# Optimization experiments

Hardware: AMD Instinct MI355X
Metric: run time of the kernel (lower is better)

## Reference

```python
import jax, jax.numpy as jnp
import numpy as np

H = W = 64          # input_resolution
C = 256             # dim
HEADS = 8
WS = 8              # window_size
SHIFT = WS // 2
DEPTH = 2           # block 0: no shift, block 1: shifted + mask
HIDDEN = 4 * C      # mlp_ratio * dim
B = 8
N = WS * WS                 # tokens per window
NW = (H // WS) * (W // WS)  # windows per image
EPS = 1e-5


def _rel_pos_index():
    coords = np.stack(np.meshgrid(np.arange(WS), np.arange(WS), indexing='ij')).reshape(2, -1)
    rel = (coords[:, :, None] - coords[:, None, :]).transpose(1, 2, 0)
    rel[:, :, 0] += WS - 1
    rel[:, :, 1] += WS - 1
    rel[:, :, 0] *= 2 * WS - 1
    return rel.sum(-1)  # [N, N] indices into (2*ws-1)^2 table

REL_IDX = jnp.asarray(_rel_pos_index())


def _attn_mask():
    # Swin shift mask: label 3x3 regions, compare window-token labels
    img = np.zeros((H, W))
    slices = (slice(0, -WS), slice(-WS, -SHIFT), slice(-SHIFT, None))
    cnt = 0
    for hs in slices:
        for ws_ in slices:
            img[hs, ws_] = cnt
            cnt += 1
    mw = img.reshape(H // WS, WS, W // WS, WS).transpose(0, 2, 1, 3).reshape(-1, N)
    diff = mw[:, None, :] - mw[:, :, None]
    return jnp.asarray(np.where(diff != 0, -100.0, 0.0), dtype=np.float32)  # [nW, N, N]

ATTN_MASK = _attn_mask()


def layernorm(x, g, b):
    mu = jnp.mean(x, axis=-1, keepdims=True)
    var = jnp.mean((x - mu) ** 2, axis=-1, keepdims=True)
    return (x - mu) * jax.lax.rsqrt(var + EPS) * g + b


def setup_inputs() -> dict:
    key = jax.random.key(0)
    ks = jax.random.split(key, 6)
    s = 0.02
    return {
        'x': jax.random.normal(ks[0], (B, H * W, C), jnp.float32),
        'qkv_w': jax.random.normal(ks[1], (DEPTH, C, 3 * C), jnp.float32) * s,
        'qkv_b': jnp.zeros((DEPTH, 3 * C), jnp.float32),
        'proj_w': jax.random.normal(ks[2], (DEPTH, C, C), jnp.float32) * s,
        'proj_b': jnp.zeros((DEPTH, C), jnp.float32),
        'ln1_g': jnp.ones((DEPTH, C), jnp.float32),
        'ln1_b': jnp.zeros((DEPTH, C), jnp.float32),
        'ln2_g': jnp.ones((DEPTH, C), jnp.float32),
        'ln2_b': jnp.zeros((DEPTH, C), jnp.float32),
        'fc1_w': jax.random.normal(ks[3], (DEPTH, C, HIDDEN), jnp.float32) * s,
        'fc1_b': jnp.zeros((DEPTH, HIDDEN), jnp.float32),
        'fc2_w': jax.random.normal(ks[4], (DEPTH, HIDDEN, C), jnp.float32) * s,
        'fc2_b': jnp.zeros((DEPTH, C), jnp.float32),
        'rpb': jax.random.normal(ks[5], (DEPTH, (2 * WS - 1) ** 2, HEADS), jnp.float32) * s,
    }


def window_attention(xw, qw, qb, pw, pb, rpb_i, mask):
    # xw: [B*nW, N, C]
    B_ = xw.shape[0]
    d = C // HEADS
    qkv = (xw @ qw + qb).reshape(B_, N, 3, HEADS, d).transpose(2, 0, 3, 1, 4)
    q, k, v = qkv[0] * (d ** -0.5), qkv[1], qkv[2]   # [B_, h, N, d]
    attn = jnp.einsum('bhnd,bhmd->bhnm', q, k)
    bias = rpb_i[REL_IDX.reshape(-1)].reshape(N, N, HEADS).transpose(2, 0, 1)
    attn = attn + bias[None]
    if mask is not None:
        attn = attn.reshape(-1, NW, HEADS, N, N) + mask[None, :, None]
        attn = attn.reshape(-1, HEADS, N, N)
    attn = jax.nn.softmax(attn, axis=-1)
    out = jnp.einsum('bhnm,bhmd->bhnd', attn, v).transpose(0, 2, 1, 3).reshape(B_, N, C)
    return out @ pw + pb


def reference(x, qkv_w, qkv_b, proj_w, proj_b, ln1_g, ln1_b, ln2_g, ln2_b,
              fc1_w, fc1_b, fc2_w, fc2_b, rpb):
    for i in range(DEPTH):
        shift = 0 if i % 2 == 0 else SHIFT
        mask = None if shift == 0 else ATTN_MASK
        shortcut = x
        h = layernorm(x, ln1_g[i], ln1_b[i]).reshape(-1, H, W, C)
        if shift:
            h = jnp.roll(h, (-shift, -shift), axis=(1, 2))
        # window partition -> [B*nW, N, C]
        hw = h.reshape(-1, H // WS, WS, W // WS, WS, C).transpose(0, 1, 3, 2, 4, 5).reshape(-1, N, C)
        aw = window_attention(hw, qkv_w[i], qkv_b[i], proj_w[i], proj_b[i], rpb[i], mask)
        # window reverse
        h = aw.reshape(-1, H // WS, W // WS, WS, WS, C).transpose(0, 1, 3, 2, 4, 5).reshape(-1, H, W, C)
        if shift:
            h = jnp.roll(h, (shift, shift), axis=(1, 2))
        x = shortcut + h.reshape(-1, H * W, C)
        m = layernorm(x, ln2_g[i], ln2_b[i])
        m = jax.nn.gelu(m @ fc1_w[i] + fc1_b[i], approximate=False) @ fc2_w[i] + fc2_b[i]
        x = x + m
    return x
```

## Files before the change

### kernel.cpp

```cpp
#include <hip/hip_runtime.h>
#include <hip/hip_bf16.h>


typedef __hip_bfloat16 bf16;
typedef unsigned short u16;
typedef unsigned int u32;
typedef short short8 __attribute__((ext_vector_type(8)));
typedef float floatx4 __attribute__((ext_vector_type(4)));

#define DEVI static __device__ __forceinline__
#define WAITCNT_VM(n) asm volatile("s_waitcnt vmcnt(" #n ")" ::: "memory")

DEVI float lo16(u32 u) { union { u32 i; float f; } x; x.i = u << 16; return x.f; }
DEVI float hi16(u32 u) { union { u32 i; float f; } x; x.i = u & 0xffff0000u; return x.f; }
DEVI float b2f(u16 u) { union { u32 i; float f; } x; x.i = ((u32)u) << 16; return x.f; }
DEVI u16 f2b(float f) {
  union { float f; u32 i; } x; x.f = f;
  u32 r = x.i + 0x7fffu + ((x.i >> 16) & 1u);
  return (u16)(r >> 16);
}
DEVI float in_elem(const void* p, size_t i, int m) {
  return m ? b2f(((const u16*)p)[i]) : ((const float*)p)[i];
}
DEVI int swlab(int g) { return (g < 56) ? 0 : (g < 60 ? 1 : 2); }

DEVI float gelu_cheap(float v) {
  const float u = v * v;
  const float t = v * __builtin_fmaf(0.1029436f, u, 2.3022090f);
  const float e = __builtin_amdgcn_exp2f(t);
  const float r = __builtin_amdgcn_rcpf(e + 1.0f);
  return __builtin_fmaf(-v, r, v);
}

DEVI void async16(const bf16* g, bf16* l) {
  __builtin_amdgcn_global_load_lds((const __attribute__((address_space(1))) u32*)g,
                                   (__attribute__((address_space(3))) u32*)l, 16, 0, 0);
}

__global__ void k_detect(const u32* __restrict__ ln1g, int* __restrict__ mode) {
  if (threadIdx.x == 0 && blockIdx.x == 0)
    *mode = (ln1g[0] == 0x3F803F80u) ? 1 : 0;
}

__global__ __launch_bounds__(256) void k_ingest_ln(const void* __restrict__ xin,
    float* __restrict__ xf, const void* __restrict__ gamw, const void* __restrict__ betw,
    bf16* __restrict__ outp, const int* __restrict__ mode)
{
  const int m = *mode;
  const int l = threadIdx.x & 63, w = threadIdx.x >> 6;
  const int row = blockIdx.x * 4 + w;
  const int t = row & 63, win = row >> 6;
  const int bb = win >> 6, wi = win & 63;
  const int gh = ((wi >> 3) << 3) + (t >> 3);
  const int gw = ((wi & 7) << 3) + (t & 7);
  const int srow = (bb << 12) + (gh << 6) + gw;
  const int cb = l << 2;
  float4 v;
  if (m) {
    const uint2 u = *(const uint2*)((const u16*)xin + (size_t)srow * 256 + cb);
    v = make_float4(lo16(u.x), hi16(u.x), lo16(u.y), hi16(u.y));
  } else {
    v = ((const float4*)((const float*)xin + (size_t)srow * 256))[l];
  }
  ((float4*)(xf + (size_t)srow * 256))[l] = v;
  float s = v.x + v.y + v.z + v.w;
#pragma unroll
  for (int off = 32; off > 0; off >>= 1) s += __shfl_xor(s, off, 64);
  const float mu = s * 0.00390625f;
  const float a = v.x - mu, b = v.y - mu, c = v.z - mu, d = v.w - mu;
  float q = a * a + b * b + c * c + d * d;
#pragma unroll
  for (int off = 32; off > 0; off >>= 1) q += __shfl_xor(q, off, 64);
  const float rs = rsqrtf(q * 0.00390625f + 1e-5f);
  const float o0 = a * rs * in_elem(gamw, cb + 0, m) + in_elem(betw, cb + 0, m);
  const float o1 = b * rs * in_elem(gamw, cb + 1, m) + in_elem(betw, cb + 1, m);
  const float o2 = c * rs * in_elem(gamw, cb + 2, m) + in_elem(betw, cb + 2, m);
  const float o3 = d * rs * in_elem(gamw, cb + 3, m) + in_elem(betw, cb + 3, m);
  const u32 p0 = (u32)f2b(o0) | ((u32)f2b(o1) << 16);
  const u32 p1 = (u32)f2b(o2) | ((u32)f2b(o3) << 16);
  *(uint2*)((u16*)outp + (size_t)row * 256 + cb) = make_uint2(p0, p1);
}

__global__ __launch_bounds__(256) void k_transpose(
    const void* __restrict__ src, bf16* __restrict__ dst,
    const int* __restrict__ mode, int estride, int dstride, int R, int Cn) {
  __shared__ float T[32][33];
  const int m = *mode;
  const int tx = threadIdx.x & 31, ty = threadIdx.x >> 5;
  const int bc = blockIdx.x << 5, br = blockIdx.y << 5;
  for (int d = 0; d < 2; ++d) {
    __syncthreads();
#pragma unroll
    for (int dy = 0; dy < 4; ++dy) {
      const int r = br + ty + dy * 8;
      T[ty + dy * 8][tx] = in_elem(src, (size_t)d * estride + (size_t)r * Cn + bc + tx, m);
    }
    __syncthreads();
#pragma unroll
    for (int dy = 0; dy < 4; ++dy) {
      const int c = bc + ty + dy * 8;
      ((u16*)dst)[(size_t)d * dstride + (size_t)c * R + br + tx] = f2b(T[tx][ty + dy * 8]);
    }
  }
}

template <int EPI>
__global__ __launch_bounds__(256, 3) void k_gemm(
    const bf16* __restrict__ A, const bf16* __restrict__ Bt,
    const void* __restrict__ bias, bf16* __restrict__ outb,
    const int* __restrict__ mode, int boff, int K, int N)
{
  __shared__ __align__(16) bf16 As[3][128 * 32];
  __shared__ __align__(16) bf16 Bs[3][128 * 32];
  __shared__ __align__(16) float EPs[4][4][72];
  const int md = *mode;
  const int tid = threadIdx.x;
  const int l = tid & 63, wid = tid >> 6;
  const int wr = wid >> 1, wc = wid & 1;

  const int gx = gridDim.x;
  const int nwg = gx * gridDim.y;
  int fid = blockIdx.y * gx + blockIdx.x;
  if (!(nwg & 7)) fid = (fid & 7) * (nwg >> 3) + (fid >> 3);
  const int row0 = (fid / gx) * 128;
  const int col0 = (fid % gx) * 128;

  const int lrow = l >> 2;
  const int lkof = (((l & 3) ^ ((l >> 3) & 3)) * 8);
  const int qsw  = (((l >> 4) ^ ((l >> 1) & 3)) * 8);

  floatx4 acc[4][4];
#pragma unroll
  for (int mi = 0; mi < 4; ++mi)
#pragma unroll
    for (int ni = 0; ni < 4; ++ni)
      acc[mi][ni] = (floatx4){0.f, 0.f, 0.f, 0.f};

  auto stage = [&](int b, int kbase) {
    const int kk = kbase + lkof;
#pragma unroll
    for (int c = 0; c < 2; ++c) {
      const int seg = c * 4 + wid;
      async16(A + (size_t)(row0 + seg * 16 + lrow) * K + kk, &As[b][seg * 512]);
      async16(Bt + (size_t)(col0 + seg * 16 + lrow) * K + kk, &Bs[b][seg * 512]);
    }
  };

  const int nsl = K >> 5;
  stage(0, 0);
  stage(1, 32);

  for (int s = 0; s < nsl; ++s) {
    const int cur = s % 3;
    if (s < nsl - 1) { WAITCNT_VM(4); }
    else            { WAITCNT_VM(0); }
    __builtin_amdgcn_s_barrier();
    if (s + 2 < nsl) stage((s + 2) % 3, (s + 2) * 32);

    short8 af[4], bq[4];
#pragma unroll
    for (int mi = 0; mi < 4; ++mi)
      af[mi] = *(const short8*)&As[cur][(wr * 64 + mi * 16 + (l & 15)) * 32 + qsw];
#pragma unroll
    for (int ni = 0; ni < 4; ++ni)
      bq[ni] = *(const short8*)&Bs[cur][(wc * 64 + ni * 16 + (l & 15)) * 32 + qsw];
#pragma unroll
    for (int mi = 0; mi < 4; ++mi)
#pragma unroll
      for (int ni = 0; ni < 4; ++ni)
        acc[mi][ni] = __builtin_amdgcn_mfma_f32_16x16x32_bf16(af[mi], bq[ni], acc[mi][ni], 0, 0, 0);
  }

  float* EPw = &EPs[wid][0][0];
  const int cl = l & 15, rq = l >> 4;
  const int colb = wc * 64 + cl * 4;
  float bias4[4];
#pragma unroll
  for (int i = 0; i < 4; ++i) bias4[i] = in_elem(bias, (size_t)boff + col0 + colb + i, md);

#pragma unroll
  for (int mi = 0; mi < 4; ++mi) {
#pragma unroll
    for (int r = 0; r < 4; ++r) {
#pragma unroll
      for (int ni = 0; ni < 4; ++ni)
        EPw[rq * 72 + ni * 16 + cl] = acc[mi][ni][r];
      const float4 av = *(const float4*)&EPw[rq * 72 + cl * 4];
      float v0 = av.x + bias4[0], v1 = av.y + bias4[1];
      float v2 = av.z + bias4[2], v3 = av.w + bias4[3];
      if (EPI == 1) {
        v0 = gelu_cheap(v0); v1 = gelu_cheap(v1);
        v2 = gelu_cheap(v2); v3 = gelu_cheap(v3);
      }
      const int row = row0 + wr * 64 + mi * 16 + rq * 4 + r;
      const u32 p0 = (u32)f2b(v0) | ((u32)f2b(v1) << 16);
      const u32 p1 = (u32)f2b(v2) | ((u32)f2b(v3) << 16);
      *(uint2*)((u16*)outb + (size_t)row * N + col0 + colb) = make_uint2(p0, p1);
    }
  }
}

template <int MODE>
__global__ __launch_bounds__(256, 2) void k_fullN(
    const bf16* __restrict__ A, const bf16* __restrict__ Bt,
    const void* __restrict__ bias, const void* __restrict__ lng,
    const void* __restrict__ lnb, void* __restrict__ outp,
    float* __restrict__ xf, const int* __restrict__ mode,
    int boff, int lnoff, int K, int shift)
{
  __shared__ __align__(16) char smem[61440];
  bf16* As = (bf16*)smem;
  bf16* Bs = (bf16*)(smem + 12288);
  const int md = *mode;
  const int tid = threadIdx.x;
  const int l = tid & 63, w = tid >> 6;

  int fid = blockIdx.x;
  const int nwg = gridDim.x;
  if (!(nwg & 7)) fid = (fid & 7) * (nwg >> 3) + (fid >> 3);
  const int row0 = fid * 64;

  const int lrow = l >> 2;
  const int lkof = (((l & 3) ^ ((l >> 3) & 3)) * 8);
  const int qsw  = (((l >> 4) ^ ((l >> 1) & 3)) * 8);

  floatx4 acc[16];
#pragma unroll
  for (int ni = 0; ni < 16; ++ni) acc[ni] = (floatx4){0.f, 0.f, 0.f, 0.f};

  auto stage = [&](int b, int kbase) {
    const int kk = kbase + lkof;
    async16(A + (size_t)(row0 + w * 16 + lrow) * K + kk, As + b * 2048 + w * 512);
#pragma unroll
    for (int c = 0; c < 4; ++c) {
      const int seg = c * 4 + w;
      async16(Bt + (size_t)(seg * 16 + lrow) * K + kk, Bs + b * 8192 + seg * 512);
    }
  };

  const int nsl = K >> 5;
  stage(0, 0);
  stage(1, 32);

  for (int s = 0; s < nsl; ++s) {
    const int cur = s % 3;
    if (s < nsl - 1) { WAITCNT_VM(5); }
    else            { WAITCNT_VM(0); }
    __builtin_amdgcn_s_barrier();
    if (s + 2 < nsl) stage((s + 2) % 3, (s + 2) * 32);

    const short8 af = *(const short8*)&As[cur * 2048 + (w * 16 + (l & 15)) * 32 + qsw];
#pragma unroll
    for (int ni = 0; ni < 16; ++ni) {
      const short8 bq = *(const short8*)&Bs[cur * 8192 + (ni * 16 + (l & 15)) * 32 + qsw];
      acc[ni] = __builtin_amdgcn_mfma_f32_16x16x32_bf16(af, bq, acc[ni], 0, 0, 0);
    }
  }

  __syncthreads();

  float* EPw = (float*)smem + w * 1088;
  const int cl = l & 15, rq = l >> 4;
  const int c4 = l * 4;

  float bias4[4], g4[4], b4[4];
#pragma unroll
  for (int i = 0; i < 4; ++i) bias4[i] = in_elem(bias, (size_t)boff + c4 + i, md);
#pragma unroll
  for (int i = 0; i < 4; ++i) {
    g4[i] = in_elem(lng, (size_t)lnoff + c4 + i, md);
    b4[i] = in_elem(lnb, (size_t)lnoff + c4 + i, md);
  }

  for (int r = 0; r < 4; ++r) {
#pragma unroll
    for (int ni = 0; ni < 16; ++ni)
      EPw[rq * 272 + ni * 16 + cl] = acc[ni][r];

#pragma unroll
    for (int g = 0; g < 4; ++g) {
      const int lrow_g = row0 + w * 16 + g * 4 + r;
      const float4 av = *(const float4*)&EPw[g * 272 + c4];

      const int t_ = lrow_g & 63, win = lrow_g >> 6;
      const int bb = win >> 6, wi2 = win & 63;
      int gh = ((wi2 >> 3) << 3) + (t_ >> 3);
      int gw = ((wi2 & 7) << 3) + (t_ & 7);
      gh = (gh + shift) & 63; gw = (gw + shift) & 63;
      const int resrow = (bb << 12) + (gh << 6) + gw;
      const int dstrow = resrow;

      const float4 xv = *(const float4*)(xf + (size_t)resrow * 256 + c4);
      float t0 = av.x + bias4[0] + xv.x;
      float t1 = av.y + bias4[1] + xv.y;
      float t2 = av.z + bias4[2] + xv.z;
      float t3 = av.w + bias4[3] + xv.w;

      float s = t0 + t1 + t2 + t3;
#pragma unroll
      for (int off = 32; off > 0; off >>= 1) s += __shfl_xor(s, off, 64);
      const float mu = s * 0.00390625f;
      const float d0 = t0 - mu, d1 = t1 - mu, d2 = t2 - mu, d3 = t3 - mu;
      float q = d0 * d0 + d1 * d1 + d2 * d2 + d3 * d3;
#pragma unroll
      for (int off = 32; off > 0; off >>= 1) q += __shfl_xor(q, off, 64);
      const float rs = rsqrtf(q * 0.00390625f + 1e-5f);

      *(float4*)(xf + (size_t)resrow * 256 + c4) = make_float4(t0, t1, t2, t3);
      const u32 p0 = (u32)f2b(d0 * rs * g4[0] + b4[0]) | ((u32)f2b(d1 * rs * g4[1] + b4[1]) << 16);
      const u32 p1 = (u32)f2b(d2 * rs * g4[2] + b4[2]) | ((u32)f2b(d3 * rs * g4[3] + b4[3]) << 16);
      *(uint2*)((u16*)outp + (size_t)dstrow * 256 + c4) = make_uint2(p0, p1);
    }
  }
}

template <int MODE>
__global__ __launch_bounds__(256) void k_mlp(
    const bf16* __restrict__ A, const bf16* __restrict__ W1t, const bf16* __restrict__ W2t,
    const void* __restrict__ b1, const void* __restrict__ b2,
    const void* __restrict__ lng, const void* __restrict__ lnb,
    void* __restrict__ outp, float* __restrict__ xf, const int* __restrict__ mode,
    int b1off, int b2off, int lnoff)
{
  __shared__ __align__(16) char smem[81920];
  bf16* Al = (bf16*)smem;
  bf16* Wl = (bf16*)(smem + 32768);
  u16*  Hl = (u16*)(smem + 65536);
  const int md = *mode;
  const int tid = threadIdx.x;
  const int l = tid & 63, w = tid >> 6;
  int fid = blockIdx.x;
  const int nwg = gridDim.x;
  if (!(nwg & 7)) fid = (fid & 7) * (nwg >> 3) + (fid >> 3);
  const int row0 = fid * 64;

  const int lr4 = l >> 2;
  const int lkof = (((l & 3) ^ ((l >> 3) & 3)) * 8);
  const int qsw  = (((l >> 4) ^ ((l >> 1) & 3)) * 8);
  const int cl = l & 15, rq = l >> 4;

  floatx4 acc2[16];
#pragma unroll
  for (int ni = 0; ni < 16; ++ni) acc2[ni] = (floatx4){0.f, 0.f, 0.f, 0.f};

  auto stageW1 = [&](int c, int s, int b) {
#pragma unroll
    for (int cc = 0; cc < 2; ++cc) {
      const int seg = w * 2 + cc;
      const size_t gr = (size_t)(c * 128 + seg * 16 + lr4) * 256;
      async16(W1t + gr + s * 32 + lkof,       Wl + b * 8192 + seg * 512);
      async16(W1t + gr + (s + 1) * 32 + lkof, Wl + b * 8192 + 4096 + seg * 512);
    }
  };
  auto stageW2 = [&](int c, int q, int b) {
#pragma unroll
    for (int cc = 0; cc < 4; ++cc) {
      const int seg = w * 4 + cc;
      async16(W2t + (size_t)(seg * 16 + lr4) * 1024 + c * 128 + q * 32 + lkof,
              Wl + b * 8192 + seg * 512);
    }
  };

#pragma unroll
  for (int s = 0; s < 8; ++s)
    async16(A + (size_t)(row0 + w * 16 + lr4) * 256 + s * 32 + lkof, Al + s * 2048 + w * 512);
  stageW1(0, 0, 0);

  int buf = 0;
  for (int c = 0; c < 8; ++c) {
    floatx4 acc1[8];
#pragma unroll
    for (int ni = 0; ni < 8; ++ni) acc1[ni] = (floatx4){0.f, 0.f, 0.f, 0.f};

    for (int p = 0; p < 4; ++p) {
      __syncthreads();
      if (p < 3) stageW1(c, 2 * (p + 1), buf ^ 1);
      else       stageW2(c, 0, buf ^ 1);
      const short8 af0 = *(const short8*)&Al[(2 * p) * 2048 + (w * 16 + cl) * 32 + qsw];
      const short8 af1 = *(const short8*)&Al[(2 * p + 1) * 2048 + (w * 16 + cl) * 32 + qsw];
#pragma unroll
      for (int ni = 0; ni < 8; ++ni) {
        const short8 bq0 = *(const short8*)(Wl + buf * 8192 + (ni * 16 + cl) * 32 + qsw);
        acc1[ni] = __builtin_amdgcn_mfma_f32_16x16x32_bf16(af0, bq0, acc1[ni], 0, 0, 0);
      }
#pragma unroll
      for (int ni = 0; ni < 8; ++ni) {
        const short8 bq1 = *(const short8*)(Wl + buf * 8192 + 4096 + (ni * 16 + cl) * 32 + qsw);
        acc1[ni] = __builtin_amdgcn_mfma_f32_16x16x32_bf16(af1, bq1, acc1[ni], 0, 0, 0);
      }
      buf ^= 1;
    }

#pragma unroll
    for (int ni = 0; ni < 8; ++ni) {
      const int hc = ni * 16 + cl;
      const float bv = in_elem(b1, (size_t)b1off + c * 128 + hc, md);
      const int hbase = (hc >> 5) * 2048;
      const int hq = (hc >> 3) & 3, he = hc & 7;
#pragma unroll
      for (int r = 0; r < 4; ++r) {
        const int hr = w * 16 + rq * 4 + r;
        Hl[hbase + hr * 32 + ((hq ^ ((hr >> 1) & 3)) * 8) + he] =
            f2b(gelu_cheap(acc1[ni][r] + bv));
      }
    }

    for (int q = 0; q < 4; ++q) {
      __syncthreads();
      if (q < 3)      stageW2(c, q + 1, buf ^ 1);
      else if (c < 7) stageW1(c + 1, 0, buf ^ 1);
      const short8 hf = *(const short8*)((const bf16*)&Hl[q * 2048 + (w * 16 + cl) * 32 + qsw]);
#pragma unroll
      for (int ni = 0; ni < 16; ++ni) {
        const short8 bq = *(const short8*)(Wl + buf * 8192 + (ni * 16 + cl) * 32 + qsw);
        acc2[ni] = __builtin_amdgcn_mfma_f32_16x16x32_bf16(hf, bq, acc2[ni], 0, 0, 0);
      }
      buf ^= 1;
    }
  }

  __syncthreads();
  float* EPw = (float*)smem + w * 1088;
  const int c4 = l * 4;

  float bias4[4], g4[4], b4[4];
#pragma unroll
  for (int i = 0; i < 4; ++i) bias4[i] = in_elem(b2, (size_t)b2off + c4 + i, md);
  if (MODE == 1) {
#pragma unroll
    for (int i = 0; i < 4; ++i) {
      g4[i] = in_elem(lng, (size_t)lnoff + c4 + i, md);
      b4[i] = in_elem(lnb, (size_t)lnoff + c4 + i, md);
    }
  }

  for (int r = 0; r < 4; ++r) {
#pragma unroll
    for (int ni = 0; ni < 16; ++ni)
      EPw[rq * 272 + ni * 16 + cl] = acc2[ni][r];

#pragma unroll
    for (int g = 0; g < 4; ++g) {
      const int lrow_g = row0 + w * 16 + g * 4 + r;
      const float4 av = *(const float4*)&EPw[g * 272 + c4];
      const float4 xv = *(const float4*)(xf + (size_t)lrow_g * 256 + c4);
      float t0 = av.x + bias4[0] + xv.x;
      float t1 = av.y + bias4[1] + xv.y;
      float t2 = av.z + bias4[2] + xv.z;
      float t3 = av.w + bias4[3] + xv.w;

      if (MODE == 2) {
        *(float4*)((float*)outp + (size_t)lrow_g * 256 + c4) = make_float4(t0, t1, t2, t3);
        continue;
      }

      const int bb = lrow_g >> 12, th = (lrow_g >> 6) & 63, tw = lrow_g & 63;
      const int gh = (th + 60) & 63, gw = (tw + 60) & 63;
      const int wi2 = ((gh >> 3) << 3) + (gw >> 3);
      const int tt = ((gh & 7) << 3) + (gw & 7);
      const int dstrow = (bb << 12) + (wi2 << 6) + tt;

      float s = t0 + t1 + t2 + t3;
#pragma unroll
      for (int off = 32; off > 0; off >>= 1) s += __shfl_xor(s, off, 64);
      const float mu = s * 0.00390625f;
      const float d0 = t0 - mu, d1 = t1 - mu, d2 = t2 - mu, d3 = t3 - mu;
      float q = d0 * d0 + d1 * d1 + d2 * d2 + d3 * d3;
#pragma unroll
      for (int off = 32; off > 0; off >>= 1) q += __shfl_xor(q, off, 64);
      const float rs = rsqrtf(q * 0.00390625f + 1e-5f);

      *(float4*)(xf + (size_t)lrow_g * 256 + c4) = make_float4(t0, t1, t2, t3);
      const u32 p0 = (u32)f2b(d0 * rs * g4[0] + b4[0]) | ((u32)f2b(d1 * rs * g4[1] + b4[1]) << 16);
      const u32 p1 = (u32)f2b(d2 * rs * g4[2] + b4[2]) | ((u32)f2b(d3 * rs * g4[3] + b4[3]) << 16);
      *(uint2*)((u16*)outp + (size_t)dstrow * 256 + c4) = make_uint2(p0, p1);
    }
  }
}

__global__ __launch_bounds__(256, 2) void k_attn(
    const bf16* __restrict__ qkv, const void* __restrict__ rpb,
    bf16* __restrict__ outp, const int* __restrict__ mode, int eoff, int shifted)
{
  __shared__ __align__(16) u16 Pl[4][64][72];
  __shared__ __align__(16) u16 Vt[4][32][72];
  __shared__ float rpbs[4][228];
  const int md = *mode;
  const int l = threadIdx.x & 63, w = threadIdx.x >> 6;
  const int cl = l & 15, qd = l >> 4;
  const int ko = qd * 8;
  const int win = blockIdx.x;
  const int wi = win & 63;
  const int whb = (wi >> 3) << 3, wwb = (wi & 7) << 3;
  const size_t rowbase = (size_t)win * 64 * 768;

  for (int hh = 0; hh < 2; ++hh) {
    const int h = w + hh * 4;
    for (int i = l; i < 225; i += 64)
      rpbs[w][i] = in_elem(rpb, (size_t)eoff + (size_t)i * 8 + h, md);
    {
      const u16* vrow = (const u16*)(qkv + rowbase + (size_t)l * 768 + 512 + h * 32);
#pragma unroll
      for (int n = 0; n < 32; ++n) Vt[w][n][l] = vrow[n];
    }
    short8 qf[4], kf[4];
#pragma unroll
    for (int t = 0; t < 4; ++t) {
      qf[t] = *(const short8*)(qkv + rowbase + (size_t)(t * 16 + cl) * 768 + h * 32 + ko);
      kf[t] = *(const short8*)(qkv + rowbase + (size_t)(t * 16 + cl) * 768 + 256 + h * 32 + ko);
    }
    __syncthreads();

    floatx4 S[4][4];
#pragma unroll
    for (int mi = 0; mi < 4; ++mi)
#pragma unroll
      for (int ni = 0; ni < 4; ++ni)
        S[mi][ni] = __builtin_amdgcn_mfma_f32_16x16x32_bf16(qf[mi], kf[ni], (floatx4){0.f, 0.f, 0.f, 0.f}, 0, 0, 0);

    int cty[4], ctx[4], clab[4];
#pragma unroll
    for (int ni = 0; ni < 4; ++ni) {
      const int ct = ni * 16 + cl;
      cty[ni] = ct >> 3; ctx[ni] = ct & 7;
      clab[ni] = shifted ? (swlab(whb + cty[ni]) * 3 + swlab(wwb + ctx[ni])) : 0;
    }

    float invs[4][4];
#pragma unroll
    for (int mi = 0; mi < 4; ++mi) {
#pragma unroll
      for (int r = 0; r < 4; ++r) {
        const int rt = mi * 16 + qd * 4 + r;
        const int rty = rt >> 3, rtx = rt & 7;
        const int rlab = shifted ? (swlab(whb + rty) * 3 + swlab(wwb + rtx)) : 0;
        float sv[4];
#pragma unroll
        for (int ni = 0; ni < 4; ++ni) {
          float x = S[mi][ni][r] * 0.17677669529663687f;
          x += rpbs[w][(rty - cty[ni] + 7) * 15 + (rtx - ctx[ni] + 7)];
          if (shifted && (rlab != clab[ni])) x -= 100.f;
          sv[ni] = x;
        }
        float mx = fmaxf(fmaxf(sv[0], sv[1]), fmaxf(sv[2], sv[3]));
        mx = fmaxf(mx, __shfl_xor(mx, 1, 64));
        mx = fmaxf(mx, __shfl_xor(mx, 2, 64));
        mx = fmaxf(mx, __shfl_xor(mx, 4, 64));
        mx = fmaxf(mx, __shfl_xor(mx, 8, 64));
        float sum = 0.f;
#pragma unroll
        for (int ni = 0; ni < 4; ++ni) { sv[ni] = __expf(sv[ni] - mx); sum += sv[ni]; }
        sum += __shfl_xor(sum, 1, 64);
        sum += __shfl_xor(sum, 2, 64);
        sum += __shfl_xor(sum, 4, 64);
        sum += __shfl_xor(sum, 8, 64);
        invs[mi][r] = __builtin_amdgcn_rcpf(sum);
#pragma unroll
        for (int ni = 0; ni < 4; ++ni) Pl[w][rt][ni * 16 + cl] = f2b(sv[ni]);
      }
    }
    __syncthreads();

    floatx4 O[4][2];
#pragma unroll
    for (int mi = 0; mi < 4; ++mi)
#pragma unroll
      for (int nv = 0; nv < 2; ++nv)
        O[mi][nv] = (floatx4){0.f, 0.f, 0.f, 0.f};
    short8 vf[2][2];
#pragma unroll
    for (int nv = 0; nv < 2; ++nv)
#pragma unroll
      for (int kk = 0; kk < 2; ++kk)
        vf[nv][kk] = *(const short8*)&Vt[w][nv * 16 + cl][kk * 32 + ko];
#pragma unroll
    for (int mi = 0; mi < 4; ++mi) {
      const short8 pf0 = *(const short8*)&Pl[w][mi * 16 + cl][ko];
      const short8 pf1 = *(const short8*)&Pl[w][mi * 16 + cl][32 + ko];
#pragma unroll
      for (int nv = 0; nv < 2; ++nv) {
        O[mi][nv] = __builtin_amdgcn_mfma_f32_16x16x32_bf16(pf0, vf[nv][0], O[mi][nv], 0, 0, 0);
        O[mi][nv] = __builtin_amdgcn_mfma_f32_16x16x32_bf16(pf1, vf[nv][1], O[mi][nv], 0, 0, 0);
      }
    }

#pragma unroll
    for (int mi = 0; mi < 4; ++mi)
#pragma unroll
      for (int nv = 0; nv < 2; ++nv)
#pragma unroll
        for (int r = 0; r < 4; ++r) {
          const int row = mi * 16 + qd * 4 + r;
          ((u16*)outp)[((size_t)win * 64 + row) * 256 + h * 32 + nv * 16 + cl] =
              f2b(O[mi][nv][r] * invs[mi][r]);
        }
    __syncthreads();
  }
}

extern "C" void kernel_launch(void* const* d_in, const int* in_sizes, int n_in,
                              void* d_out, int out_size, void* d_ws, size_t ws_size,
                              hipStream_t stream) {
  (void)in_sizes; (void)n_in; (void)out_size; (void)ws_size;
  const void* x_in   = d_in[0];
  const void* qkv_w  = d_in[1];
  const void* qkv_b  = d_in[2];
  const void* proj_w = d_in[3];
  const void* proj_b = d_in[4];
  const void* ln1_g  = d_in[5];
  const void* ln1_b  = d_in[6];
  const void* ln2_g  = d_in[7];
  const void* ln2_b  = d_in[8];
  const void* fc1_w  = d_in[9];
  const void* fc1_b  = d_in[10];
  const void* fc2_w  = d_in[11];
  const void* fc2_b  = d_in[12];
  const void* rpb    = d_in[13];

  char* ws = (char*)d_ws;
  float* xf  = (float*)ws;
  bf16* bufQ = (bf16*)(ws + 100663296);
  bf16* bufB = (bf16*)(ws + 150994944);
  bf16* wT   = (bf16*)(ws + 167772160);
  int* mode  = (int*)(ws + 170917888);

  k_detect<<<1, 1, 0, stream>>>((const u32*)ln1_g, mode);
  k_ingest_ln<<<8192, 256, 0, stream>>>(x_in, xf, ln1_g, ln1_b, bufB, mode);

  k_transpose<<<dim3(24, 8), 256, 0, stream>>>(qkv_w,  wT,          mode, 196608, 786432, 256, 768);
  k_transpose<<<dim3(8, 8), 256, 0, stream>>>(proj_w, wT + 196608, mode, 65536, 786432, 256, 256);
  k_transpose<<<dim3(32, 8), 256, 0, stream>>>(fc1_w, wT + 262144, mode, 262144, 786432, 256, 1024);
  k_transpose<<<dim3(8, 32), 256, 0, stream>>>(fc2_w, wT + 524288, mode, 262144, 786432, 1024, 256);

  for (int i = 0; i < 2; ++i) {
    const int shift = i ? 4 : 0;
    bf16* base  = wT + (size_t)i * 786432;
    bf16* qkvT  = base;
    bf16* projT = base + 196608;
    bf16* fc1T  = base + 262144;
    bf16* fc2T  = base + 524288;

    k_gemm<0><<<dim3(6, 256), 256, 0, stream>>>(bufB, qkvT, qkv_b, bufQ, mode, i * 768, 256, 768);
    k_attn<<<512, 256, 0, stream>>>(bufQ, rpb, bufB, mode, i * 1800, i);
    k_fullN<0><<<512, 256, 0, stream>>>(bufB, projT, proj_b, ln2_g, ln2_b, bufQ, xf, mode,
                                        i * 256, i * 256, 256, shift);
    if (i == 0)
      k_mlp<1><<<512, 256, 0, stream>>>(bufQ, fc1T, fc2T, fc1_b, fc2_b, ln1_g, ln1_b,
                                        bufB, xf, mode, 0, 0, 256);
    else
      k_mlp<2><<<512, 256, 0, stream>>>(bufQ, fc1T, fc2T, fc1_b, fc2_b, nullptr, nullptr,
                                        d_out, xf, mode, 1024, 256, 0);
  }
}
```

Measured before the change: 421.2 us.

## Repartition fused MLP warps to split output columns instead of rows

Switches the fused MLP kernel's per-wave work split. Previously each wave owned 16 rows and all output columns. Now each wave owns all 64 rows and a column slice: 32 hidden columns in the first GEMM and 64 output columns in the second. Each B-operand fragment loaded from shared memory is now reused across four MFMAs, which cuts LDS traffic for weights, at the cost of more A-fragment loads per wave. The hidden tile is written per-wave into its own slice. The epilogue now goes through a full-tile shared-memory transpose with an extra barrier, so each wave can still process 16 whole rows for the LayerNorm.

```diff
diff --git a/kernel.cpp b/kernel.cpp
--- a/kernel.cpp
+++ b/kernel.cpp
@@ -339,9 +339,12 @@
   const int qsw  = (((l >> 4) ^ ((l >> 1) & 3)) * 8);
   const int cl = l & 15, rq = l >> 4;
 
-  floatx4 acc2[16];
-#pragma unroll
-  for (int ni = 0; ni < 16; ++ni) acc2[ni] = (floatx4){0.f, 0.f, 0.f, 0.f};
+  floatx4 acc2[4][4];
+#pragma unroll
+  for (int mi = 0; mi < 4; ++mi)
+#pragma unroll
+    for (int ni = 0; ni < 4; ++ni)
+      acc2[mi][ni] = (floatx4){0.f, 0.f, 0.f, 0.f};
 
   auto stageW1 = [&](int c, int s, int b) {
 #pragma unroll
@@ -368,61 +371,83 @@
 
   int buf = 0;
   for (int c = 0; c < 8; ++c) {
-    floatx4 acc1[8];
-#pragma unroll
-    for (int ni = 0; ni < 8; ++ni) acc1[ni] = (floatx4){0.f, 0.f, 0.f, 0.f};
+    floatx4 acc1[4][2];
+#pragma unroll
+    for (int mi = 0; mi < 4; ++mi)
+#pragma unroll
+      for (int bni = 0; bni < 2; ++bni)
+        acc1[mi][bni] = (floatx4){0.f, 0.f, 0.f, 0.f};
 
     for (int p = 0; p < 4; ++p) {
       __syncthreads();
       if (p < 3) stageW1(c, 2 * (p + 1), buf ^ 1);
       else       stageW2(c, 0, buf ^ 1);
-      const short8 af0 = *(const short8*)&Al[(2 * p) * 2048 + (w * 16 + cl) * 32 + qsw];
-      const short8 af1 = *(const short8*)&Al[(2 * p + 1) * 2048 + (w * 16 + cl) * 32 + qsw];
-#pragma unroll
-      for (int ni = 0; ni < 8; ++ni) {
-        const short8 bq0 = *(const short8*)(Wl + buf * 8192 + (ni * 16 + cl) * 32 + qsw);
-        acc1[ni] = __builtin_amdgcn_mfma_f32_16x16x32_bf16(af0, bq0, acc1[ni], 0, 0, 0);
-      }
-#pragma unroll
-      for (int ni = 0; ni < 8; ++ni) {
-        const short8 bq1 = *(const short8*)(Wl + buf * 8192 + 4096 + (ni * 16 + cl) * 32 + qsw);
-        acc1[ni] = __builtin_amdgcn_mfma_f32_16x16x32_bf16(af1, bq1, acc1[ni], 0, 0, 0);
+#pragma unroll
+      for (int h2 = 0; h2 < 2; ++h2) {
+        const int ks = 2 * p + h2;
+        short8 af[4];
+#pragma unroll
+        for (int mi = 0; mi < 4; ++mi)
+          af[mi] = *(const short8*)&Al[ks * 2048 + (mi * 16 + cl) * 32 + qsw];
+#pragma unroll
+        for (int bni = 0; bni < 2; ++bni) {
+          const short8 bq = *(const short8*)(Wl + buf * 8192 + h2 * 4096 +
+                                             (w * 32 + bni * 16 + cl) * 32 + qsw);
+#pragma unroll
+          for (int mi = 0; mi < 4; ++mi)
+            acc1[mi][bni] = __builtin_amdgcn_mfma_f32_16x16x32_bf16(af[mi], bq, acc1[mi][bni], 0, 0, 0);
+        }
       }
       buf ^= 1;
     }
 
 #pragma unroll
-    for (int ni = 0; ni < 8; ++ni) {
-      const int hc = ni * 16 + cl;
-      const float bv = in_elem(b1, (size_t)b1off + c * 128 + hc, md);
-      const int hbase = (hc >> 5) * 2048;
-      const int hq = (hc >> 3) & 3, he = hc & 7;
-#pragma unroll
-      for (int r = 0; r < 4; ++r) {
-        const int hr = w * 16 + rq * 4 + r;
-        Hl[hbase + hr * 32 + ((hq ^ ((hr >> 1) & 3)) * 8) + he] =
-            f2b(gelu_cheap(acc1[ni][r] + bv));
-      }
+    for (int bni = 0; bni < 2; ++bni) {
+      const int hcl = w * 32 + bni * 16 + cl;
+      const float bv = in_elem(b1, (size_t)b1off + c * 128 + hcl, md);
+      const int hq = (hcl >> 3) & 3, he = hcl & 7;
+#pragma unroll
+      for (int mi = 0; mi < 4; ++mi)
+#pragma unroll
+        for (int r = 0; r < 4; ++r) {
+          const int hr = mi * 16 + rq * 4 + r;
+          Hl[w * 2048 + hr * 32 + ((hq ^ ((hr >> 1) & 3)) * 8) + he] =
+              f2b(gelu_cheap(acc1[mi][bni][r] + bv));
+        }
     }
 
     for (int q = 0; q < 4; ++q) {
       __syncthreads();
       if (q < 3)      stageW2(c, q + 1, buf ^ 1);
       else if (c < 7) stageW1(c + 1, 0, buf ^ 1);
-      const short8 hf = *(const short8*)((const bf16*)&Hl[q * 2048 + (w * 16 + cl) * 32 + qsw]);
-#pragma unroll
-      for (int ni = 0; ni < 16; ++ni) {
-        const short8 bq = *(const short8*)(Wl + buf * 8192 + (ni * 16 + cl) * 32 + qsw);
-        acc2[ni] = __builtin_amdgcn_mfma_f32_16x16x32_bf16(hf, bq, acc2[ni], 0, 0, 0);
+      short8 hf[4];
+#pragma unroll
+      for (int mi = 0; mi < 4; ++mi)
+        hf[mi] = *(const short8*)((const bf16*)&Hl[q * 2048 + (mi * 16 + cl) * 32 + qsw]);
+#pragma unroll
+      for (int ni = 0; ni < 4; ++ni) {
+        const short8 bq = *(const short8*)(Wl + buf * 8192 +
+                                           (w * 64 + ni * 16 + cl) * 32 + qsw);
+#pragma unroll
+        for (int mi = 0; mi < 4; ++mi)
+          acc2[mi][ni] = __builtin_amdgcn_mfma_f32_16x16x32_bf16(hf[mi], bq, acc2[mi][ni], 0, 0, 0);
       }
       buf ^= 1;
     }
   }
 
   __syncthreads();
-  float* EPw = (float*)smem + w * 1088;
+  float* EPf = (float*)smem;
+#pragma unroll
+  for (int mi = 0; mi < 4; ++mi)
+#pragma unroll
+    for (int ni = 0; ni < 4; ++ni)
+#pragma unroll
+      for (int r = 0; r < 4; ++r)
+        EPf[(mi * 16 + rq * 4 + r) * 272 + w * 64 + ni * 16 + cl] = acc2[mi][ni][r];
+  __syncthreads();
+
   const int c4 = l * 4;
-
   float bias4[4], g4[4], b4[4];
 #pragma unroll
   for (int i = 0; i < 4; ++i) bias4[i] = in_elem(b2, (size_t)b2off + c4 + i, md);
@@ -434,47 +459,40 @@
     }
   }
 
-  for (int r = 0; r < 4; ++r) {
-#pragma unroll
-    for (int ni = 0; ni < 16; ++ni)
-      EPw[rq * 272 + ni * 16 + cl] = acc2[ni][r];
-
-#pragma unroll
-    for (int g = 0; g < 4; ++g) {
-      const int lrow_g = row0 + w * 16 + g * 4 + r;
-      const float4 av = *(const float4*)&EPw[g * 272 + c4];
-      const float4 xv = *(const float4*)(xf + (size_t)lrow_g * 256 + c4);
-      float t0 = av.x + bias4[0] + xv.x;
-      float t1 = av.y + bias4[1] + xv.y;
-      float t2 = av.z + bias4[2] + xv.z;
-      float t3 = av.w + bias4[3] + xv.w;
-
-      if (MODE == 2) {
-        *(float4*)((float*)outp + (size_t)lrow_g * 256 + c4) = make_float4(t0, t1, t2, t3);
-        continue;
-      }
-
-      const int bb = lrow_g >> 12, th = (lrow_g >> 6) & 63, tw = lrow_g & 63;
-      const int gh = (th + 60) & 63, gw = (tw + 60) & 63;
-      const int wi2 = ((gh >> 3) << 3) + (gw >> 3);
-      const int tt = ((gh & 7) << 3) + (gw & 7);
-      const int dstrow = (bb << 12) + (wi2 << 6) + tt;
-
-      float s = t0 + t1 + t2 + t3;
-#pragma unroll
-      for (int off = 32; off > 0; off >>= 1) s += __shfl_xor(s, off, 64);
-      const float mu = s * 0.00390625f;
-      const float d0 = t0 - mu, d1 = t1 - mu, d2 = t2 - mu, d3 = t3 - mu;
-      float q = d0 * d0 + d1 * d1 + d2 * d2 + d3 * d3;
-#pragma unroll
-      for (int off = 32; off > 0; off >>= 1) q += __shfl_xor(q, off, 64);
-      const float rs = rsqrtf(q * 0.00390625f + 1e-5f);
-
-      *(float4*)(xf + (size_t)lrow_g * 256 + c4) = make_float4(t0, t1, t2, t3);
-      const u32 p0 = (u32)f2b(d0 * rs * g4[0] + b4[0]) | ((u32)f2b(d1 * rs * g4[1] + b4[1]) << 16);
-      const u32 p1 = (u32)f2b(d2 * rs * g4[2] + b4[2]) | ((u32)f2b(d3 * rs * g4[3] + b4[3]) << 16);
-      *(uint2*)((u16*)outp + (size_t)dstrow * 256 + c4) = make_uint2(p0, p1);
-    }
+  for (int rr = 0; rr < 16; ++rr) {
+    const int lrow_g = row0 + w * 16 + rr;
+    const float4 av = *(const float4*)&EPf[(w * 16 + rr) * 272 + c4];
+    const float4 xv = *(const float4*)(xf + (size_t)lrow_g * 256 + c4);
+    float t0 = av.x + bias4[0] + xv.x;
+    float t1 = av.y + bias4[1] + xv.y;
+    float t2 = av.z + bias4[2] + xv.z;
+    float t3 = av.w + bias4[3] + xv.w;
+
+    if (MODE == 2) {
+      *(float4*)((float*)outp + (size_t)lrow_g * 256 + c4) = make_float4(t0, t1, t2, t3);
+      continue;
+    }
+
+    const int bb = lrow_g >> 12, th = (lrow_g >> 6) & 63, tw = lrow_g & 63;
+    const int gh = (th + 60) & 63, gw = (tw + 60) & 63;
+    const int wi2 = ((gh >> 3) << 3) + (gw >> 3);
+    const int tt = ((gh & 7) << 3) + (gw & 7);
+    const int dstrow = (bb << 12) + (wi2 << 6) + tt;
+
+    float s = t0 + t1 + t2 + t3;
+#pragma unroll
+    for (int off = 32; off > 0; off >>= 1) s += __shfl_xor(s, off, 64);
+    const float mu = s * 0.00390625f;
+    const float d0 = t0 - mu, d1 = t1 - mu, d2 = t2 - mu, d3 = t3 - mu;
+    float q = d0 * d0 + d1 * d1 + d2 * d2 + d3 * d3;
+#pragma unroll
+    for (int off = 32; off > 0; off >>= 1) q += __shfl_xor(q, off, 64);
+    const float rs = rsqrtf(q * 0.00390625f + 1e-5f);
+
+    *(float4*)(xf + (size_t)lrow_g * 256 + c4) = make_float4(t0, t1, t2, t3);
+    const u32 p0 = (u32)f2b(d0 * rs * g4[0] + b4[0]) | ((u32)f2b(d1 * rs * g4[1] + b4[1]) << 16);
+    const u32 p1 = (u32)f2b(d2 * rs * g4[2] + b4[2]) | ((u32)f2b(d3 * rs * g4[3] + b4[3]) << 16);
+    *(uint2*)((u16*)outp + (size_t)dstrow * 256 + c4) = make_uint2(p0, p1);
   }
 }
 
```

Measured after the change: 399.0 us. 1.06x faster.
